# Optimization experiments

Measured on AMD Instinct MI355X. Metric: run time of the kernel, lower is better.

## Reference

```python
import jax, jax.numpy as jnp
import numpy as np

# ---- static config (matches init_kwargs and NSA hyperparams in source) ----
DIM = 512; HEADS = 8; DH = DIM // HEADS; DEPTH = 2
HH = 28; WW = 28; SEQ = HH * WW            # 784
WIN = 28 * 7                                # sliding window = 196
CBS = 28 * 14; CST = 28 * 7                 # compress block 392, stride 196
SBS = 28 * 14; NSEL = 1                     # selection block 392, top-1
NC = (SEQ - CBS) // CST + 1                 # 3 compressed blocks
NS = SEQ // SBS                             # 2 selection blocks
EPS = 1e-5
BATCH = 8


def _overlap_matrix():
    # fraction of each compressed block overlapping each selection block
    O = np.zeros((NC, NS), np.float32)
    for i in range(NC):
        a, b = i * CST, i * CST + CBS
        for j in range(NS):
            c, d = j * SBS, (j + 1) * SBS
            O[i, j] = max(0, min(b, d) - max(a, c)) / CBS
    return jnp.asarray(O)

OVERLAP = _overlap_matrix()  # [NC, NS]


def setup_inputs() -> dict:
    key = jax.random.key(0)
    ks = jax.random.split(key, 12)
    p = lambda i, shape, s=0.02: (jax.random.normal(ks[i], shape, jnp.float32) * s)
    return {
        "x": jax.random.normal(ks[0], (BATCH, DIM, HH, WW), jnp.float32),
        "pos_emb": jax.random.normal(ks[1], (SEQ,), jnp.float32),
        "attn_norm_g": jnp.ones((DEPTH, DIM), jnp.float32),
        "Wq": p(2, (DEPTH, DIM, HEADS * DH)),
        "Wk": p(3, (DEPTH, DIM, HEADS * DH)),
        "Wv": p(4, (DEPTH, DIM, HEADS * DH)),
        "Wo": p(5, (DEPTH, HEADS * DH, DIM)),
        "Wg": p(6, (DEPTH, DIM, HEADS * 3)),
        "ff_norm_g": jnp.ones((DEPTH, DIM), jnp.float32),
        "ff_norm_b": jnp.zeros((DEPTH, DIM), jnp.float32),
        "ff_w1": p(7, (DEPTH, 4 * DIM, DIM)),
        "ff_b1": jnp.zeros((DEPTH, 4 * DIM), jnp.float32),
        "ff_w2": p(8, (DEPTH, DIM, 4 * DIM)),
        "ff_b2": jnp.zeros((DEPTH, DIM), jnp.float32),
    }


def _sparse_attn(x, g, wq, wk, wv, wo, wg):
    # x: [b, n, d]  -- NSA: sliding window + compressed + top-k block selection
    b, n, d = x.shape
    xr = x * jax.lax.rsqrt(jnp.mean(x * x, -1, keepdims=True) + EPS) * g  # RMSNorm
    q = (xr @ wq).reshape(b, n, HEADS, DH)
    k = (xr @ wk).reshape(b, n, HEADS, DH)
    v = (xr @ wv).reshape(b, n, HEADS, DH)
    scale = DH ** -0.5

    # ---- compressed branch: mean-pool overlapping blocks ----
    ck = jnp.stack([k[:, i * CST:i * CST + CBS].mean(1) for i in range(NC)], 1)  # [b,NC,h,dh]
    cv = jnp.stack([v[:, i * CST:i * CST + CBS].mean(1) for i in range(NC)], 1)
    sc = jnp.einsum('bihd,bjhd->bhij', q, ck) * scale          # [b,h,n,NC]
    pc = jax.nn.softmax(sc, -1)
    out_c = jnp.einsum('bhij,bjhd->bihd', pc, cv)              # [b,n,h,dh]

    # ---- selection branch: importance -> top-k selection blocks -> fine attn ----
    imp = jnp.einsum('bhij,jk->bhik', pc, OVERLAP)             # [b,h,n,NS]
    _, sel = jax.lax.top_k(imp, NSEL)                          # [b,h,n,NSEL]
    selmask = jax.nn.one_hot(sel, NS, dtype=jnp.float32).sum(-2) > 0  # [b,h,n,NS]
    blk = jnp.arange(n) // SBS                                 # token -> selection block
    tokmask = selmask[..., blk]                                # [b,h,n,n]
    sf = jnp.einsum('bihd,bjhd->bhij', q, k) * scale           # full fine scores (shared)
    neg = jnp.finfo(sf.dtype).min
    ps = jax.nn.softmax(jnp.where(tokmask, sf, neg), -1)
    out_s = jnp.einsum('bhij,bjhd->bihd', ps, v)

    # ---- sliding window branch ----
    idx = jnp.arange(n)
    winmask = jnp.abs(idx[:, None] - idx[None, :]) < WIN       # [n,n]
    pw = jax.nn.softmax(jnp.where(winmask, sf, neg), -1)
    out_w = jnp.einsum('bhij,bjhd->bihd', pw, v)

    # ---- per-head learned gates over the 3 branches ----
    gates = jax.nn.sigmoid(xr @ wg).reshape(b, n, HEADS, 3)
    o = (gates[..., 0:1] * out_c + gates[..., 1:2] * out_s + gates[..., 2:3] * out_w)
    return o.reshape(b, n, HEADS * DH) @ wo


def _ff(x, g, bb, w1, b1, w2, b2):
    # x: [b,c,h,w]; LayerNorm over channel dim, then 1x1 conv -> GELU -> 1x1 conv
    mean = x.mean(1, keepdims=True)
    var = jnp.var(x, 1, keepdims=True)
    xn = (x - mean) / jnp.sqrt(var + EPS) * g[None, :, None, None] + bb[None, :, None, None]
    h1 = jax.nn.gelu(jnp.einsum('bchw,oc->bohw', xn, w1) + b1[None, :, None, None], approximate=False)
    return jnp.einsum('bchw,oc->bohw', h1, w2) + b2[None, :, None, None]


def reference(x, pos_emb, attn_norm_g, Wq, Wk, Wv, Wo, Wg,
              ff_norm_g, ff_norm_b, ff_w1, ff_b1, ff_w2, ff_b2):
    b, c, h, w = x.shape
    x = x + pos_emb[:h * w].reshape(1, 1, h, w)
    for l in range(DEPTH):
        s = x.reshape(b, c, h * w).transpose(0, 2, 1)          # b (h w) c
        s = _sparse_attn(s, attn_norm_g[l], Wq[l], Wk[l], Wv[l], Wo[l], Wg[l]) + s
        x = s.transpose(0, 2, 1).reshape(b, c, h, w)
        x = _ff(x, ff_norm_g[l], ff_norm_b[l], ff_w1[l], ff_b1[l], ff_w2[l], ff_b2[l]) + x
    return x
```

## Files before the change

kernel.cpp:

```cpp
#include <hip/hip_runtime.h>
#include <hip/hip_bf16.h>
#include <math.h>

#define B_      8
#define DIMC    512
#define SEQ_    784
#define HEADS_  8
#define DH_     64
#define NTOK    (B_*SEQ_)
#define QLD     1560
#define WIN_    196
#define CBS_    392
#define CST_    196
#define NC_     3
#define EPSF    1e-5f
#define FF_     2048
#define TQ_     28
#define MT_     98

typedef __hip_bfloat16 bf16_t;
typedef __attribute__((ext_vector_type(8))) short bf16x8;
typedef __attribute__((ext_vector_type(4))) float floatx4;
typedef __attribute__((ext_vector_type(4))) unsigned int uintx4;
typedef __attribute__((ext_vector_type(2))) unsigned int uintx2;

__device__ __forceinline__ float wsum(float x){
#pragma unroll
  for (int o = 32; o; o >>= 1) x += __shfl_xor(x, o, 64);
  return x;
}
__device__ __forceinline__ float geluf(float x){
  return 0.5f * x * (1.0f + erff(x * 0.70710678118654752f));
}
__device__ __forceinline__ float sigmoidf_(float x){
  return 1.0f / (1.0f + __expf(-x));
}
__device__ __forceinline__ void gload16(const bf16_t* g, bf16_t* l){
  __builtin_amdgcn_global_load_lds(
      (const __attribute__((address_space(1))) void*)g,
      (__attribute__((address_space(3))) void*)l, 16, 0, 0);
}

__global__ __launch_bounds__(256) void k_init(const float* __restrict__ xin,
                                              const float* __restrict__ pos,
                                              float* __restrict__ X){
  __shared__ float tl[32][33];
  int blk = blockIdx.x;
  int ct = blk & 15;
  int pt = (blk >> 4) % 25;
  int b  = blk / (16 * 25);
  int p0 = pt * 32, c0 = ct * 32;
  int tx = threadIdx.x & 31, ty = threadIdx.x >> 5;
#pragma unroll
  for (int i = 0; i < 4; i++){
    int p = p0 + tx;
    if (p < SEQ_) tl[ty + i * 8][tx] = xin[((long)(b * DIMC + c0 + ty + i * 8)) * SEQ_ + p];
  }
  __syncthreads();
#pragma unroll
  for (int i = 0; i < 4; i++){
    int p = p0 + ty + i * 8;
    if (p < SEQ_)
      X[((long)(b * SEQ_ + p)) * DIMC + c0 + tx] = tl[tx][ty + i * 8] + pos[p];
  }
}

__global__ __launch_bounds__(256) void k_final(const float* __restrict__ X,
                                               float* __restrict__ out){
  __shared__ float tl[32][33];
  int blk = blockIdx.x;
  int ct = blk & 15;
  int pt = (blk >> 4) % 25;
  int b  = blk / (16 * 25);
  int p0 = pt * 32, c0 = ct * 32;
  int tx = threadIdx.x & 31, ty = threadIdx.x >> 5;
#pragma unroll
  for (int i = 0; i < 4; i++){
    int p = p0 + ty + i * 8;
    if (p < SEQ_) tl[ty + i * 8][tx] = X[((long)(b * SEQ_ + p)) * DIMC + c0 + tx];
  }
  __syncthreads();
#pragma unroll
  for (int i = 0; i < 4; i++){
    int p = p0 + tx;
    if (p < SEQ_)
      out[((long)(b * DIMC + c0 + ty + i * 8)) * SEQ_ + p] = tl[tx][ty + i * 8];
  }
}

__global__ __launch_bounds__(256) void k_wconv1(const float* __restrict__ Wq,
                                                const float* __restrict__ Wk,
                                                const float* __restrict__ Wv,
                                                const float* __restrict__ Wg,
                                                bf16_t* __restrict__ Wb){
  __shared__ float tl[32][33];
  int blk = blockIdx.x;
  int kt = blk & 15;
  int ntf = (blk >> 4) % 49;
  int l = blk / (16 * 49);
  int n0 = ntf * 32, k0 = kt * 32;
  int tx = threadIdx.x & 31, ty = threadIdx.x >> 5;
#pragma unroll
  for (int i = 0; i < 4; i++){
    int n = n0 + tx, k = k0 + ty + i * 8;
    float v = 0.0f;
    if (n < 1536){
      int which = n >> 9, nn = n & 511;
      const float* W = (which == 0) ? Wq : ((which == 1) ? Wk : Wv);
      v = W[((long)(l * 512 + k)) * 512 + nn];
    } else if (n < QLD){
      v = Wg[((long)(l * 512 + k)) * 24 + (n - 1536)];
    }
    tl[ty + i * 8][tx] = v;
  }
  __syncthreads();
#pragma unroll
  for (int i = 0; i < 4; i++){
    int n = n0 + ty + i * 8, k = k0 + tx;
    if (n < QLD)
      Wb[((long)(l * QLD + n)) * 512 + k] = __float2bfloat16(tl[tx][ty + i * 8]);
  }
}

__global__ __launch_bounds__(256) void k_wconv2(const float* __restrict__ Wo,
                                                bf16_t* __restrict__ Wb){
  __shared__ float tl[32][33];
  int blk = blockIdx.x;
  int kt = blk & 15;
  int ntf = (blk >> 4) & 15;
  int l = blk >> 8;
  int n0 = ntf * 32, k0 = kt * 32;
  int tx = threadIdx.x & 31, ty = threadIdx.x >> 5;
#pragma unroll
  for (int i = 0; i < 4; i++)
    tl[ty + i * 8][tx] = Wo[((long)(l * 512 + k0 + ty + i * 8)) * 512 + n0 + tx];
  __syncthreads();
#pragma unroll
  for (int i = 0; i < 4; i++)
    Wb[((long)(l * 512 + n0 + ty + i * 8)) * 512 + k0 + tx] = __float2bfloat16(tl[tx][ty + i * 8]);
}

__global__ __launch_bounds__(256) void k_cast(const float* __restrict__ src,
                                              bf16_t* __restrict__ dst){
  int idx = blockIdx.x * 256 + threadIdx.x;
  dst[idx] = __float2bfloat16(src[idx]);
}

__global__ __launch_bounds__(256) void k_zero(uintx4* __restrict__ p){
  p[blockIdx.x * 256 + threadIdx.x] = (uintx4){0u, 0u, 0u, 0u};
}

__global__ __launch_bounds__(256) void k_rms(const float* __restrict__ X,
                                             const float* __restrict__ g,
                                             bf16_t* __restrict__ XR){
  int tok = blockIdx.x;
  int tid = threadIdx.x;
  const float* xr = X + (long)tok * DIMC;
  float v0 = xr[tid], v1 = xr[tid + 256];
  float ss = v0 * v0 + v1 * v1;
  ss = wsum(ss);
  __shared__ float red[4];
  if ((tid & 63) == 0) red[tid >> 6] = ss;
  __syncthreads();
  float tot = red[0] + red[1] + red[2] + red[3];
  float r = rsqrtf(tot * (1.0f / DIMC) + EPSF);
  XR[(long)tok * DIMC + tid]       = __float2bfloat16(v0 * r * g[tid]);
  XR[(long)tok * DIMC + tid + 256] = __float2bfloat16(v1 * r * g[tid + 256]);
}

__global__ __launch_bounds__(256) void k_ln(const float* __restrict__ X,
                                            const float* __restrict__ g,
                                            const float* __restrict__ bb,
                                            bf16_t* __restrict__ XN){
  int tok = blockIdx.x;
  int tid = threadIdx.x;
  const float* xr = X + (long)tok * DIMC;
  float v0 = xr[tid], v1 = xr[tid + 256];
  float s = v0 + v1;
  float q = v0 * v0 + v1 * v1;
  s = wsum(s); q = wsum(q);
  __shared__ float r1[4], r2[4];
  if ((tid & 63) == 0){ r1[tid >> 6] = s; r2[tid >> 6] = q; }
  __syncthreads();
  float ts = r1[0] + r1[1] + r1[2] + r1[3];
  float tq = r2[0] + r2[1] + r2[2] + r2[3];
  float mean = ts * (1.0f / DIMC);
  float var  = tq * (1.0f / DIMC) - mean * mean;
  float rinv = rsqrtf(var + EPSF);
  XN[(long)tok * DIMC + tid]       = __float2bfloat16((v0 - mean) * rinv * g[tid]       + bb[tid]);
  XN[(long)tok * DIMC + tid + 256] = __float2bfloat16((v1 - mean) * rinv * g[tid + 256] + bb[tid + 256]);
}

template<int OUTBF, int ACT, int TN, int BK>
__global__ __launch_bounds__(256) void k_mgemm(const bf16_t* __restrict__ A,
                                               const bf16_t* __restrict__ Bm,
                                               float* Cf,
                                               bf16_t* Cb,
                                               const float* __restrict__ bias,
                                               const float* res,
                                               int M, int N, int K, int ldc, int ccol,
                                               bf16_t* VTo){
  constexpr int NTW  = TN / 2;
  constexpr int NF   = TN / 32;
  constexpr int KS   = BK / 32;
  constexpr int RPB2 = 512 / BK;
  constexpr int LPR  = BK / 8;
  constexpr int ABLK = BK / 8;
  constexpr int BBLK = (TN * BK) / 512;
  constexpr int TOT  = ABLK + BBLK;
  constexpr int PW   = TOT / 4;
  static_assert(TOT % 4 == 0, "stage blocks must split across 4 waves");

  int id = blockIdx.x;
  int xcd = id & 7;
  int j = id >> 3;
  int nt = j / 13;
  int mt = xcd * 13 + (j - nt * 13);
  if (mt >= MT_) return;
  int bm = mt * 64, bn = nt * TN;

  __shared__ bf16_t As[2][64][BK];
  __shared__ bf16_t Bs[2][TN][BK];
  int tid = threadIdx.x;
  int w = tid >> 6, lane = tid & 63;
  int wm = (w & 1) * 32, wn = (w >> 1) * NTW;
  int quad = lane >> 4, l16 = lane & 15;

  int lr = lane / LPR, lc = (lane % LPR) * 8;
  const bf16_t* gsrc[PW];
  bf16_t* ldst0[PW];
  bf16_t* ldst1[PW];
#pragma unroll
  for (int i = 0; i < PW; i++){
    int bi = w * PW + i;
    if (bi < ABLK){
      gsrc[i]  = A + (long)(bm + bi * RPB2 + lr) * K + lc;
      ldst0[i] = &As[0][bi * RPB2][0];
      ldst1[i] = &As[1][bi * RPB2][0];
    } else {
      int bj = bi - ABLK;
      int r = bn + bj * RPB2 + lr; if (r >= N) r = N - 1;
      gsrc[i]  = Bm + (long)r * K + lc;
      ldst0[i] = &Bs[0][bj * RPB2][0];
      ldst1[i] = &Bs[1][bj * RPB2][0];
    }
  }

  floatx4 acc[2][NF];
#pragma unroll
  for (int i = 0; i < 2; i++)
#pragma unroll
    for (int jj = 0; jj < NF; jj++) acc[i][jj] = (floatx4)(0.0f);

#define MG_STAGE0(ko) do { _Pragma("unroll") \
    for (int i_ = 0; i_ < PW; i_++) gload16(gsrc[i_] + (ko), ldst0[i_]); } while (0)
#define MG_STAGE1(ko) do { _Pragma("unroll") \
    for (int i_ = 0; i_ < PW; i_++) gload16(gsrc[i_] + (ko), ldst1[i_]); } while (0)
#define MG_COMPUTE(BUFI) do { _Pragma("unroll") \
    for (int ks_ = 0; ks_ < KS; ks_++){ \
      bf16x8 a0_ = *(bf16x8*)&As[BUFI][wm + l16][ks_ * 32 + quad * 8]; \
      bf16x8 a1_ = *(bf16x8*)&As[BUFI][wm + 16 + l16][ks_ * 32 + quad * 8]; \
      bf16x8 bf_[NF]; \
      _Pragma("unroll") \
      for (int f_ = 0; f_ < NF; f_++) \
        bf_[f_] = *(bf16x8*)&Bs[BUFI][wn + f_ * 16 + l16][ks_ * 32 + quad * 8]; \
      _Pragma("unroll") \
      for (int f_ = 0; f_ < NF; f_++){ \
        acc[0][f_] = __builtin_amdgcn_mfma_f32_16x16x32_bf16(a0_, bf_[f_], acc[0][f_], 0, 0, 0); \
        acc[1][f_] = __builtin_amdgcn_mfma_f32_16x16x32_bf16(a1_, bf_[f_], acc[1][f_], 0, 0, 0); \
      } \
    } } while (0)

  int nch = K / BK;
  MG_STAGE0(0);
  __syncthreads();
  for (int ch = 0; ch < nch; ch += 2){
    MG_STAGE1((ch + 1) * BK);
    MG_COMPUTE(0);
    __syncthreads();
    if (ch + 2 < nch) MG_STAGE0((ch + 2) * BK);
    MG_COMPUTE(1);
    __syncthreads();
  }
#undef MG_STAGE0
#undef MG_STAGE1
#undef MG_COMPUTE

#pragma unroll
  for (int tm = 0; tm < 2; tm++){
#pragma unroll
    for (int tn = 0; tn < NF; tn++){
      int ncol = bn + wn + tn * 16 + l16;
      if (ncol >= N) continue;
#pragma unroll
      for (int reg = 0; reg < 4; reg++){
        long mrow = bm + wm + tm * 16 + quad * 4 + reg;
        float v = acc[tm][tn][reg];
        if (bias) v += bias[ncol];
        if (ACT == 1) v = geluf(v);
        long off = mrow * (long)ldc + ccol + ncol;
        if (res) v += res[off];
        if (OUTBF){
          Cb[off] = __float2bfloat16(v);
          if (VTo && ncol >= 1024 && ncol < 1536){
            int bb2 = (int)(mrow / SEQ_);
            int tok = (int)(mrow - (long)bb2 * SEQ_);
            VTo[((long)(bb2 * 512 + (ncol - 1024))) * 800 + tok] = __float2bfloat16(v);
          }
        }
        else       Cf[off] = v;
      }
    }
  }
}

__global__ __launch_bounds__(512) void k_cpool(const bf16_t* __restrict__ qkvg,
                                               float* __restrict__ ck,
                                               float* __restrict__ cv){
  int bj = blockIdx.x;
  int j = bj % NC_;
  int b = bj / NC_;
  int tid = threadIdx.x;
  int seg = tid & 127;
  int rg  = tid >> 7;
  __shared__ float part[4][1024];
  const bf16_t* base = qkvg + ((long)b * SEQ_ + (long)j * CST_) * QLD + 512;
  float acc[8] = {0.f,0.f,0.f,0.f,0.f,0.f,0.f,0.f};
  for (int r = rg; r < CBS_; r += 4){
    uintx4 v = *(const uintx4*)(base + (long)r * QLD + seg * 8);
    bf16_t tmp[8]; *(uintx4*)tmp = v;
#pragma unroll
    for (int q = 0; q < 8; q++) acc[q] += __bfloat162float(tmp[q]);
  }
#pragma unroll
  for (int q = 0; q < 8; q++) part[rg][seg * 8 + q] = acc[q];
  __syncthreads();
  for (int c = tid; c < 1024; c += 512){
    float s = (part[0][c] + part[1][c]) + (part[2][c] + part[3][c]);
    s *= (1.0f / CBS_);
    if (c < 512) ck[bj * DIMC + c] = s;
    else         cv[bj * DIMC + (c - 512)] = s;
  }
}

__global__ __launch_bounds__(256) void k_attn(const bf16_t* __restrict__ qkvg,
                                              const float* __restrict__ ck,
                                              const float* __restrict__ cv,
                                              const bf16_t* __restrict__ vtg,
                                              bf16_t* __restrict__ oattn){
  int tid = threadIdx.x;
  int w = tid >> 6, lane = tid & 63;
  int quad = lane >> 4, l16 = lane & 15;
  int id = blockIdx.x;
  int xcd = id & 7;
  int j = id >> 3;
  int bh = xcd * 8 + (j / 28);
  int i0 = (j % 28) * TQ_;
  int h = bh & 7, b = bh >> 3;
  const float scale = 0.125f;

  __shared__ bf16_t Qs[32][72];
  __shared__ bf16_t Ks[2][64][72];
  __shared__ bf16_t Wcw[2][32][72];
  __shared__ bf16_t Wcs[2][32][72];
  __shared__ float outc_s[28][64];
  __shared__ int   sel_s[28];
  __shared__ float cw_s[28], cs_s[28], g1_s[28], g2_s[28];
  __shared__ float red_s[4][4][16];

  const long rowBase = (long)b * SEQ_ * QLD + h * 64;

  if (tid < 224){
    int q = tid >> 3, seg = tid & 7;
    uintx4 qv = *(const uintx4*)(qkvg + rowBase + (long)(i0 + q) * QLD + seg * 8);
    *(uintx4*)&Qs[q][seg * 8] = qv;
  } else {
    int u = tid - 224;
    int r = 28 + (u >> 3), seg = u & 7;
    *(uintx4*)&Qs[r][seg * 8] = (uintx4){0u, 0u, 0u, 0u};
  }
  for (int t = tid; t < 2 * 4 * 72; t += 256){
    int bufi = t / (4 * 72);
    int r = 28 + (t / 72) % 4;
    int c = t % 72;
    Wcw[bufi][r][c] = __float2bfloat16(0.0f);
    Wcs[bufi][r][c] = __float2bfloat16(0.0f);
  }
  __syncthreads();

  int r0i = tid >> 3, s0i = tid & 7;
  int r1i = 32 + r0i;
  uintx4 kreg0 = *(const uintx4*)(qkvg + rowBase + (long)r0i * QLD + 512 + s0i * 8);
  uintx4 kreg1 = *(const uintx4*)(qkvg + rowBase + (long)r1i * QLD + 512 + s0i * 8);

  {
    const float* CKp = ck + (long)b * NC_ * DIMC + h * 64 + lane;
    const float* CVp = cv + (long)b * NC_ * DIMC + h * 64 + lane;
    float k0 = CKp[0], k1 = CKp[512], k2 = CKp[1024];
    float v0 = CVp[0], v1 = CVp[512], v2 = CVp[1024];
#pragma unroll
    for (int qp = 0; qp < 7; qp++){
      int qg = w * 7 + qp;
      float qd = __bfloat162float(Qs[qg][lane]);
      float s0 = wsum(qd * k0) * scale;
      float s1 = wsum(qd * k1) * scale;
      float s2 = wsum(qd * k2) * scale;
      float m3 = fmaxf(s0, fmaxf(s1, s2));
      float e0 = __expf(s0 - m3), e1 = __expf(s1 - m3), e2 = __expf(s2 - m3);
      float inv = 1.0f / (e0 + e1 + e2);
      const bf16_t* grow = qkvg + (long)(b * SEQ_ + i0 + qg) * QLD + 1536 + h * 3;
      float g0 = sigmoidf_(__bfloat162float(grow[0]));
      float g1v = sigmoidf_(__bfloat162float(grow[1]));
      float g2v = sigmoidf_(__bfloat162float(grow[2]));
      outc_s[qg][lane] = g0 * (e0 * v0 + e1 * v1 + e2 * v2) * inv;
      int selv = (s2 > s0) ? 1 : 0;
      if (lane == 0){ sel_s[qg] = selv; g1_s[qg] = g1v; g2_s[qg] = g2v; }
    }
  }

  bf16x8 a00 = *(bf16x8*)&Qs[l16][quad * 8];
  bf16x8 a01 = *(bf16x8*)&Qs[l16][32 + quad * 8];
  bf16x8 a10 = *(bf16x8*)&Qs[16 + l16][quad * 8];
  bf16x8 a11 = *(bf16x8*)&Qs[16 + l16][32 + quad * 8];

  __syncthreads();

  int nsel1 = 0;
#pragma unroll
  for (int q = 0; q < 28; q++) nsel1 += sel_s[q];
  const bool any0 = (nsel1 < 28), any1 = (nsel1 > 0);

  int sel0i = sel_s[l16];
  int sel1i = (l16 < 12) ? sel_s[16 + l16] : 0;
  bool sv0 = (sel0i != 0), sv1 = (sel1i != 0);
  int iq0 = i0 + l16, iq1 = i0 + 16 + l16;
  float sw0 = 0.f, ss0 = 0.f, sw1 = 0.f, ss1 = 0.f;

  const bf16_t* vbase = vtg + ((long)(b * 512 + h * 64 + w * 16 + l16)) * 800;
  floatx4 ow0 = (floatx4)(0.0f), ow1 = (floatx4)(0.0f);
  floatx4 os0 = (floatx4)(0.0f), os1 = (floatx4)(0.0f);

  for (int ch = 0; ch < 13; ch++){
    int buf = ch & 1;
    int K0 = ch * 64;
    bool wact = (K0 + 63 >= i0 - 195) && (K0 <= i0 + 222);
    bool sact = ((K0 <= 391) && any0) || ((K0 + 63 >= 392) && any1);
    bool pact = wact || sact;
    *(uintx4*)&Ks[buf][r0i][s0i * 8] = kreg0;
    *(uintx4*)&Ks[buf][r1i][s0i * 8] = kreg1;
    __syncthreads();
    if (ch + 1 < 13){
      int c0n = (ch + 1) * 64;
      int t0 = c0n + r0i; if (t0 > 783) t0 = 783;
      int t1 = c0n + r1i; if (t1 > 783) t1 = 783;
      kreg0 = *(const uintx4*)(qkvg + rowBase + (long)t0 * QLD + 512 + s0i * 8);
      kreg1 = *(const uintx4*)(qkvg + rowBase + (long)t1 * QLD + 512 + s0i * 8);
    }
    int tv0 = K0 + quad * 8;      if (tv0 > 792) tv0 = 792;
    int tv1 = K0 + 32 + quad * 8; if (tv1 > 792) tv1 = 792;
    bf16x8 bv0 = *(const bf16x8*)(vbase + tv0);
    bf16x8 bv1 = *(const bf16x8*)(vbase + tv1);
    if (pact){
      bf16x8 k0 = *(bf16x8*)&Ks[buf][w * 16 + l16][quad * 8];
      bf16x8 k1 = *(bf16x8*)&Ks[buf][w * 16 + l16][32 + quad * 8];
      floatx4 d0 = (floatx4)(0.0f), d1 = (floatx4)(0.0f);
      d0 = __builtin_amdgcn_mfma_f32_16x16x32_bf16(k0, a00, d0, 0, 0, 0);
      d0 = __builtin_amdgcn_mfma_f32_16x16x32_bf16(k1, a01, d0, 0, 0, 0);
      d1 = __builtin_amdgcn_mfma_f32_16x16x32_bf16(k0, a10, d1, 0, 0, 0);
      d1 = __builtin_amdgcn_mfma_f32_16x16x32_bf16(k1, a11, d1, 0, 0, 0);
      int kb = K0 + w * 16 + quad * 4;
      float ex0[4], ex1[4];
#pragma unroll
      for (int r = 0; r < 4; r++){
        ex0[r] = __expf(d0[r] * scale);
        ex1[r] = __expf(d1[r] * scale);
      }
      int kloc = w * 16 + quad * 4;
      if (wact){
        union { bf16_t hh[4]; uintx2 v; } pw0, pw1;
#pragma unroll
        for (int r = 0; r < 4; r++){
          int key = kb + r;
          bool valid = key < 784;
          float vw0 = (valid && key >= iq0 - 195 && key <= iq0 + 195) ? ex0[r] : 0.0f;
          float vw1 = (valid && key >= iq1 - 195 && key <= iq1 + 195) ? ex1[r] : 0.0f;
          sw0 += vw0; sw1 += vw1;
          pw0.hh[r] = __float2bfloat16(vw0);
          pw1.hh[r] = __float2bfloat16(vw1);
        }
        if (kb < 784){
          *(uintx2*)&Wcw[buf][l16][kloc] = pw0.v;
          if (l16 < 12) *(uintx2*)&Wcw[buf][16 + l16][kloc] = pw1.v;
        }
      }
      if (sact){
        union { bf16_t hh[4]; uintx2 v; } ps0, ps1;
#pragma unroll
        for (int r = 0; r < 4; r++){
          int key = kb + r;
          bool valid = key < 784;
          float vs0 = (valid && ((key >= 392) == sv0)) ? ex0[r] : 0.0f;
          float vs1 = (valid && ((key >= 392) == sv1)) ? ex1[r] : 0.0f;
          ss0 += vs0; ss1 += vs1;
          ps0.hh[r] = __float2bfloat16(vs0);
          ps1.hh[r] = __float2bfloat16(vs1);
        }
        if (kb < 784){
          *(uintx2*)&Wcs[buf][l16][kloc] = ps0.v;
          if (l16 < 12) *(uintx2*)&Wcs[buf][16 + l16][kloc] = ps1.v;
        }
      }
    }
    __syncthreads();
    if (wact){
#pragma unroll
      for (int ks = 0; ks < 2; ks++){
        bf16x8 bv = ks ? bv1 : bv0;
        bf16x8 aw0 = *(bf16x8*)&Wcw[buf][l16][ks * 32 + quad * 8];
        bf16x8 aw1 = *(bf16x8*)&Wcw[buf][16 + l16][ks * 32 + quad * 8];
        ow0 = __builtin_amdgcn_mfma_f32_16x16x32_bf16(aw0, bv, ow0, 0, 0, 0);
        ow1 = __builtin_amdgcn_mfma_f32_16x16x32_bf16(aw1, bv, ow1, 0, 0, 0);
      }
    }
    if (sact){
#pragma unroll
      for (int ks = 0; ks < 2; ks++){
        bf16x8 bv = ks ? bv1 : bv0;
        bf16x8 as0 = *(bf16x8*)&Wcs[buf][l16][ks * 32 + quad * 8];
        bf16x8 as1 = *(bf16x8*)&Wcs[buf][16 + l16][ks * 32 + quad * 8];
        os0 = __builtin_amdgcn_mfma_f32_16x16x32_bf16(as0, bv, os0, 0, 0, 0);
        os1 = __builtin_amdgcn_mfma_f32_16x16x32_bf16(as1, bv, os1, 0, 0, 0);
      }
    }
  }

  sw0 += __shfl_xor(sw0, 16, 64); sw0 += __shfl_xor(sw0, 32, 64);
  ss0 += __shfl_xor(ss0, 16, 64); ss0 += __shfl_xor(ss0, 32, 64);
  sw1 += __shfl_xor(sw1, 16, 64); sw1 += __shfl_xor(sw1, 32, 64);
  ss1 += __shfl_xor(ss1, 16, 64); ss1 += __shfl_xor(ss1, 32, 64);
  if (quad == 0){
    red_s[w][0][l16] = sw0; red_s[w][1][l16] = ss0;
    red_s[w][2][l16] = sw1; red_s[w][3][l16] = ss1;
  }
  __syncthreads();
  if (tid < 28){
    int q = tid, t = q >> 4, l = q & 15;
    float sw = 0.f, ss = 0.f;
#pragma unroll
    for (int wv = 0; wv < 4; wv++){ sw += red_s[wv][2 * t][l]; ss += red_s[wv][2 * t + 1][l]; }
    cw_s[q] = g2_s[q] / sw;
    cs_s[q] = g1_s[q] / ss;
  }
  __syncthreads();

  int d = w * 16 + l16;
#pragma unroll
  for (int reg = 0; reg < 4; reg++){
    int q = quad * 4 + reg;
    float o = cw_s[q] * ow0[reg] + cs_s[q] * os0[reg] + outc_s[q][d];
    oattn[((long)(b * SEQ_ + i0 + q)) * DIMC + h * 64 + d] = __float2bfloat16(o);
    int q2 = q + 16;
    if (q2 < 28){
      float o2 = cw_s[q2] * ow1[reg] + cs_s[q2] * os1[reg] + outc_s[q2][d];
      oattn[((long)(b * SEQ_ + i0 + q2)) * DIMC + h * 64 + d] = __float2bfloat16(o2);
    }
  }
}

extern "C" void kernel_launch(void* const* d_in, const int* in_sizes, int n_in,
                              void* d_out, int out_size, void* d_ws, size_t ws_size,
                              hipStream_t stream){
  const float* xin  = (const float*)d_in[0];
  const float* pos  = (const float*)d_in[1];
  const float* angm = (const float*)d_in[2];
  const float* Wq   = (const float*)d_in[3];
  const float* Wk   = (const float*)d_in[4];
  const float* Wv   = (const float*)d_in[5];
  const float* Wo   = (const float*)d_in[6];
  const float* Wg   = (const float*)d_in[7];
  const float* fng  = (const float*)d_in[8];
  const float* fnb  = (const float*)d_in[9];
  const float* fw1  = (const float*)d_in[10];
  const float* fb1  = (const float*)d_in[11];
  const float* fw2  = (const float*)d_in[12];
  const float* fb2  = (const float*)d_in[13];

  char* cw = (char*)d_ws;
  float* X = (float*)cw;             cw += (long)NTOK * 512 * 4;
  bf16_t* XRb = (bf16_t*)cw;         cw += (long)NTOK * 512 * 2;
  bf16_t* OAb = (bf16_t*)cw;         cw += (long)NTOK * 512 * 2;
  bf16_t* SH  = (bf16_t*)cw;         cw += (long)NTOK * FF_ * 2;
  float* CK = (float*)cw;            cw += (long)B_ * NC_ * DIMC * 4;
  float* CV = (float*)cw;            cw += (long)B_ * NC_ * DIMC * 4;
  bf16_t* Wqkvgb = (bf16_t*)cw;      cw += (long)2 * QLD * 512 * 2;
  bf16_t* WOb    = (bf16_t*)cw;      cw += (long)2 * 512 * 512 * 2;
  bf16_t* FW1b   = (bf16_t*)cw;      cw += (long)2 * FF_ * 512 * 2;
  bf16_t* FW2b   = (bf16_t*)cw;      cw += (long)2 * 512 * FF_ * 2;
  bf16_t* VTb    = (bf16_t*)cw;      cw += (long)B_ * 512 * 800 * 2;
  bf16_t* BUFb = SH;
  bf16_t* H1b  = SH;

  k_wconv1<<<2 * 49 * 16, 256, 0, stream>>>(Wq, Wk, Wv, Wg, Wqkvgb);
  k_wconv2<<<2 * 16 * 16, 256, 0, stream>>>(Wo, WOb);
  k_cast<<<(2 * FF_ * 512) / 256, 256, 0, stream>>>(fw1, FW1b);
  k_cast<<<(2 * 512 * FF_) / 256, 256, 0, stream>>>(fw2, FW2b);

  k_zero<<<1600, 256, 0, stream>>>((uintx4*)VTb);

  k_init<<<8 * 25 * 16, 256, 0, stream>>>(xin, pos, X);

  for (int l = 0; l < 2; l++){
    k_rms<<<NTOK, 256, 0, stream>>>(X, angm + (long)l * DIMC, XRb);

    k_mgemm<1, 0, 128, 32><<<13 * 104, 256, 0, stream>>>(
        XRb, Wqkvgb + (long)l * QLD * 512, nullptr, BUFb, nullptr, nullptr,
        NTOK, QLD, 512, QLD, 0, VTb);

    k_cpool<<<B_ * NC_, 512, 0, stream>>>(BUFb, CK, CV);

    k_attn<<<8 * 8 * 28, 256, 0, stream>>>(BUFb, CK, CV, VTb, OAb);

    k_mgemm<0, 0, 64, 64><<<8 * 104, 256, 0, stream>>>(
        OAb, WOb + (long)l * 512 * 512, X, nullptr, nullptr, X,
        NTOK, 512, 512, 512, 0, nullptr);

    k_ln<<<NTOK, 256, 0, stream>>>(X, fng + (long)l * DIMC, fnb + (long)l * DIMC, XRb);

    k_mgemm<1, 1, 128, 32><<<16 * 104, 256, 0, stream>>>(
        XRb, FW1b + (long)l * FF_ * 512, nullptr, H1b, fb1 + (long)l * FF_, nullptr,
        NTOK, FF_, 512, FF_, 0, nullptr);
    k_mgemm<0, 0, 64, 64><<<8 * 104, 256, 0, stream>>>(
        H1b, FW2b + (long)l * 512 * FF_, X, nullptr, fb2 + (long)l * DIMC, X,
        NTOK, 512, FF_, 512, 0, nullptr);
  }

  k_final<<<8 * 25 * 16, 256, 0, stream>>>(X, (float*)d_out);
}
```

Before: 577.6 us.

## Enlarge GEMM M-tile to 128 for wide GEMMs and split compressed pooling across channels

```diff
diff --git a/kernel.cpp b/kernel.cpp
--- a/kernel.cpp
+++ b/kernel.cpp
@@ -16,7 +16,6 @@
 #define EPSF    1e-5f
 #define FF_     2048
 #define TQ_     28
-#define MT_     98
 
 typedef __hip_bfloat16 bf16_t;
 typedef __attribute__((ext_vector_type(8))) short bf16x8;
@@ -191,21 +190,23 @@
   XN[(long)tok * DIMC + tid + 256] = __float2bfloat16((v1 - mean) * rinv * g[tid + 256] + bb[tid + 256]);
 }
 
-template<int OUTBF, int ACT, int TN, int BK>
+template<int OUTBF, int ACT, int BM, int TN, int BK>
 __global__ __launch_bounds__(256) void k_mgemm(const bf16_t* __restrict__ A,
                                                const bf16_t* __restrict__ Bm,
                                                float* Cf,
                                                bf16_t* Cb,
                                                const float* __restrict__ bias,
                                                const float* res,
-                                               int M, int N, int K, int ldc, int ccol,
+                                               int N, int K, int ldc,
                                                bf16_t* VTo){
-  constexpr int NTW  = TN / 2;
+  constexpr int MTILES = NTOK / BM;
+  constexpr int MPX  = (MTILES + 7) / 8;
+  constexpr int MF   = BM / 32;
   constexpr int NF   = TN / 32;
   constexpr int KS   = BK / 32;
   constexpr int RPB2 = 512 / BK;
   constexpr int LPR  = BK / 8;
-  constexpr int ABLK = BK / 8;
+  constexpr int ABLK = (BM * BK) / 512;
   constexpr int BBLK = (TN * BK) / 512;
   constexpr int TOT  = ABLK + BBLK;
   constexpr int PW   = TOT / 4;
@@ -214,16 +215,16 @@
   int id = blockIdx.x;
   int xcd = id & 7;
   int j = id >> 3;
-  int nt = j / 13;
-  int mt = xcd * 13 + (j - nt * 13);
-  if (mt >= MT_) return;
-  int bm = mt * 64, bn = nt * TN;
-
-  __shared__ bf16_t As[2][64][BK];
+  int nt = j / MPX;
+  int mt = xcd * MPX + (j - nt * MPX);
+  if (mt >= MTILES) return;
+  int bm = mt * BM, bn = nt * TN;
+
+  __shared__ bf16_t As[2][BM][BK];
   __shared__ bf16_t Bs[2][TN][BK];
   int tid = threadIdx.x;
   int w = tid >> 6, lane = tid & 63;
-  int wm = (w & 1) * 32, wn = (w >> 1) * NTW;
+  int wm = (w & 1) * (BM / 2), wn = (w >> 1) * (TN / 2);
   int quad = lane >> 4, l16 = lane & 15;
 
   int lr = lane / LPR, lc = (lane % LPR) * 8;
@@ -246,9 +247,9 @@
     }
   }
 
-  floatx4 acc[2][NF];
-#pragma unroll
-  for (int i = 0; i < 2; i++)
+  floatx4 acc[MF][NF];
+#pragma unroll
+  for (int i = 0; i < MF; i++)
 #pragma unroll
     for (int jj = 0; jj < NF; jj++) acc[i][jj] = (floatx4)(0.0f);
 
@@ -258,17 +259,18 @@
     for (int i_ = 0; i_ < PW; i_++) gload16(gsrc[i_] + (ko), ldst1[i_]); } while (0)
 #define MG_COMPUTE(BUFI) do { _Pragma("unroll") \
     for (int ks_ = 0; ks_ < KS; ks_++){ \
-      bf16x8 a0_ = *(bf16x8*)&As[BUFI][wm + l16][ks_ * 32 + quad * 8]; \
-      bf16x8 a1_ = *(bf16x8*)&As[BUFI][wm + 16 + l16][ks_ * 32 + quad * 8]; \
-      bf16x8 bf_[NF]; \
+      bf16x8 af_[MF], bf_[NF]; \
+      _Pragma("unroll") \
+      for (int m_ = 0; m_ < MF; m_++) \
+        af_[m_] = *(bf16x8*)&As[BUFI][wm + m_ * 16 + l16][ks_ * 32 + quad * 8]; \
       _Pragma("unroll") \
       for (int f_ = 0; f_ < NF; f_++) \
         bf_[f_] = *(bf16x8*)&Bs[BUFI][wn + f_ * 16 + l16][ks_ * 32 + quad * 8]; \
       _Pragma("unroll") \
-      for (int f_ = 0; f_ < NF; f_++){ \
-        acc[0][f_] = __builtin_amdgcn_mfma_f32_16x16x32_bf16(a0_, bf_[f_], acc[0][f_], 0, 0, 0); \
-        acc[1][f_] = __builtin_amdgcn_mfma_f32_16x16x32_bf16(a1_, bf_[f_], acc[1][f_], 0, 0, 0); \
-      } \
+      for (int m_ = 0; m_ < MF; m_++) \
+        _Pragma("unroll") \
+        for (int f_ = 0; f_ < NF; f_++) \
+          acc[m_][f_] = __builtin_amdgcn_mfma_f32_16x16x32_bf16(af_[m_], bf_[f_], acc[m_][f_], 0, 0, 0); \
     } } while (0)
 
   int nch = K / BK;
@@ -287,7 +289,7 @@
 #undef MG_COMPUTE
 
 #pragma unroll
-  for (int tm = 0; tm < 2; tm++){
+  for (int tm = 0; tm < MF; tm++){
 #pragma unroll
     for (int tn = 0; tn < NF; tn++){
       int ncol = bn + wn + tn * 16 + l16;
@@ -298,7 +300,7 @@
         float v = acc[tm][tn][reg];
         if (bias) v += bias[ncol];
         if (ACT == 1) v = geluf(v);
-        long off = mrow * (long)ldc + ccol + ncol;
+        long off = mrow * (long)ldc + ncol;
         if (res) v += res[off];
         if (OUTBF){
           Cb[off] = __float2bfloat16(v);
@@ -314,19 +316,21 @@
   }
 }
 
-__global__ __launch_bounds__(512) void k_cpool(const bf16_t* __restrict__ qkvg,
+__global__ __launch_bounds__(256) void k_cpool(const bf16_t* __restrict__ qkvg,
                                                float* __restrict__ ck,
                                                float* __restrict__ cv){
-  int bj = blockIdx.x;
+  int blk = blockIdx.x;
+  int cs = blk & 7;
+  int bj = blk >> 3;
   int j = bj % NC_;
   int b = bj / NC_;
   int tid = threadIdx.x;
-  int seg = tid & 127;
-  int rg  = tid >> 7;
-  __shared__ float part[4][1024];
-  const bf16_t* base = qkvg + ((long)b * SEQ_ + (long)j * CST_) * QLD + 512;
+  int seg = tid & 15;
+  int rg  = tid >> 4;
+  __shared__ float part[16][128];
+  const bf16_t* base = qkvg + ((long)b * SEQ_ + (long)j * CST_) * QLD + 512 + cs * 128;
   float acc[8] = {0.f,0.f,0.f,0.f,0.f,0.f,0.f,0.f};
-  for (int r = rg; r < CBS_; r += 4){
+  for (int r = rg; r < CBS_; r += 16){
     uintx4 v = *(const uintx4*)(base + (long)r * QLD + seg * 8);
     bf16_t tmp[8]; *(uintx4*)tmp = v;
 #pragma unroll
@@ -335,11 +339,14 @@
 #pragma unroll
   for (int q = 0; q < 8; q++) part[rg][seg * 8 + q] = acc[q];
   __syncthreads();
-  for (int c = tid; c < 1024; c += 512){
-    float s = (part[0][c] + part[1][c]) + (part[2][c] + part[3][c]);
+  if (tid < 128){
+    float s = 0.f;
+#pragma unroll
+    for (int g = 0; g < 16; g++) s += part[g][tid];
     s *= (1.0f / CBS_);
-    if (c < 512) ck[bj * DIMC + c] = s;
-    else         cv[bj * DIMC + (c - 512)] = s;
+    int gch = cs * 128 + tid;
+    if (gch < 512) ck[bj * DIMC + gch] = s;
+    else           cv[bj * DIMC + (gch - 512)] = s;
   }
 }
 
@@ -612,26 +619,26 @@
   for (int l = 0; l < 2; l++){
     k_rms<<<NTOK, 256, 0, stream>>>(X, angm + (long)l * DIMC, XRb);
 
-    k_mgemm<1, 0, 128, 32><<<13 * 104, 256, 0, stream>>>(
+    k_mgemm<1, 0, 128, 128, 32><<<13 * 56, 256, 0, stream>>>(
         XRb, Wqkvgb + (long)l * QLD * 512, nullptr, BUFb, nullptr, nullptr,
-        NTOK, QLD, 512, QLD, 0, VTb);
-
-    k_cpool<<<B_ * NC_, 512, 0, stream>>>(BUFb, CK, CV);
+        QLD, 512, QLD, VTb);
+
+    k_cpool<<<B_ * NC_ * 8, 256, 0, stream>>>(BUFb, CK, CV);
 
     k_attn<<<8 * 8 * 28, 256, 0, stream>>>(BUFb, CK, CV, VTb, OAb);
 
-    k_mgemm<0, 0, 64, 64><<<8 * 104, 256, 0, stream>>>(
+    k_mgemm<0, 0, 64, 64, 64><<<8 * 104, 256, 0, stream>>>(
         OAb, WOb + (long)l * 512 * 512, X, nullptr, nullptr, X,
-        NTOK, 512, 512, 512, 0, nullptr);
+        512, 512, 512, nullptr);
 
     k_ln<<<NTOK, 256, 0, stream>>>(X, fng + (long)l * DIMC, fnb + (long)l * DIMC, XRb);
 
-    k_mgemm<1, 1, 128, 32><<<16 * 104, 256, 0, stream>>>(
+    k_mgemm<1, 1, 128, 128, 32><<<16 * 56, 256, 0, stream>>>(
         XRb, FW1b + (long)l * FF_ * 512, nullptr, H1b, fb1 + (long)l * FF_, nullptr,
-        NTOK, FF_, 512, FF_, 0, nullptr);
-    k_mgemm<0, 0, 64, 64><<<8 * 104, 256, 0, stream>>>(
+        FF_, 512, FF_, nullptr);
+    k_mgemm<0, 0, 64, 64, 64><<<8 * 104, 256, 0, stream>>>(
         H1b, FW2b + (long)l * 512 * FF_, X, nullptr, fb2 + (long)l * DIMC, X,
-        NTOK, 512, FF_, 512, 0, nullptr);
+        512, FF_, 512, nullptr);
   }
 
   k_final<<<8 * 25 * 16, 256, 0, stream>>>(X, (float*)d_out);
```

Measured after the change: 580.1 us. Within noise of the previous version (+0.4%).
